# Kernel optimization log

Measured on AMD Instinct MI355X. Metric: run time of the kernel, lower is better.

Reference implementation:

```python
import jax, jax.numpy as jnp
import numpy as np

THR = 0.2
POOL_A = 160
POOL_B = 96
EPS = 1e-5


def _adaptive_avg_pool_last(x, out_size):
    # torch AdaptiveAvgPool1d semantics: bin i averages [floor(i*n/o), ceil((i+1)*n/o))
    n = x.shape[-1]
    i = np.arange(out_size)
    starts = (i * n) // out_size
    ends = -((-(i + 1) * n) // out_size)
    cs = jnp.cumsum(x, axis=-1)
    cs = jnp.concatenate([jnp.zeros_like(cs[..., :1]), cs], axis=-1)
    sums = cs[..., ends] - cs[..., starts]
    return sums / jnp.asarray(ends - starts, x.dtype)


def _unfold3x3(x, H, W):
    # Faithful to torch: raw reshape (N, L, C) -> (N, C, H, W) (memory reinterpretation,
    # NOT a transpose), then F.unfold(k=3, pad=1) and rearrange 'n (c ww) l -> n l ww c'.
    N, L, C = x.shape
    img = x.reshape(N, C, H, W)
    pad = jnp.pad(img, ((0, 0), (0, 0), (1, 1), (1, 1)))
    # window positions in row-major (ky, kx) order, matching F.unfold
    patches = jnp.stack([pad[:, :, dy:dy + H, dx:dx + W]
                         for dy in range(3) for dx in range(3)], axis=2)  # (N,C,9,H,W)
    return patches.transpose(0, 3, 4, 2, 1).reshape(N, H * W, 9, C)  # (N,L,9,C)


def _forward(feat_s0, feat_s1, ln_weight, ln_bias):
    N, L, C = feat_s0.shape
    H = W = int(round(L ** 0.5))
    conf = jnp.einsum('nlc,nsc->nls', feat_s0, feat_s1) / (C ** 0.5)
    conf = jax.nn.softmax(conf, axis=1) * jax.nn.softmax(conf, axis=2)
    # mutual nearest-neighbor mask with confidence threshold
    mask = ((conf > THR)
            & (conf == conf.max(axis=2, keepdims=True))
            & (conf == conf.max(axis=1, keepdims=True))).astype(feat_s0.dtype)
    u0 = _unfold3x3(feat_s0, H, W)
    u1 = _unfold3x3(feat_s1, H, W)
    sem0 = jnp.einsum('nlc,nlwc->nlw', feat_s0, u0) / C  # divided by C (shape[-1]), as in source
    sem1 = jnp.einsum('nlc,nlwc->nlw', feat_s1, u1) / C
    fea0 = jnp.einsum('nlwc,nlw->nlc', u0, sem0)
    fea1 = jnp.einsum('nlwc,nlw->nlc', u1, sem1)
    s0 = jnp.einsum('nls,nsd->nld', mask, fea1) / L
    s1 = jnp.einsum('nsl,nsd->nld', mask, fea0) / L
    f0 = jnp.concatenate([_adaptive_avg_pool_last(feat_s0, POOL_A),
                          _adaptive_avg_pool_last(s0, POOL_B)], axis=-1)
    f1 = jnp.concatenate([_adaptive_avg_pool_last(feat_s1, POOL_A),
                          _adaptive_avg_pool_last(s1, POOL_B)], axis=-1)
    f = jnp.concatenate([f0, f1], axis=0)  # (2N, L, 256)
    mu = f.mean(-1, keepdims=True)
    var = f.var(-1, keepdims=True)
    f = (f - mu) * jax.lax.rsqrt(var + EPS) * ln_weight + ln_bias
    return f[:N], f[N:]


def setup_inputs():
    key = jax.random.key(0)
    k0, k1 = jax.random.split(key)
    N, L, C = 2, 4096, 256
    return {
        'feat_s0': jax.random.normal(k0, (N, L, C), jnp.float32),
        'feat_s1': jax.random.normal(k1, (N, L, C), jnp.float32),
        'ln_weight': jnp.ones((C,), jnp.float32),
        'ln_bias': jnp.zeros((C,), jnp.float32),
    }


def reference(feat_s0, feat_s1, ln_weight, ln_bias):
    return _forward(feat_s0, feat_s1, ln_weight, ln_bias)
```

## Files before the change

kernel.cpp:

```cpp
#include <hip/hip_runtime.h>
#include <stdint.h>

#define NBATCH 2
#define LL 4096
#define CC 256
#define LSTR8 144
#define KEXP 0.09016844f
#define KEXP2 0.18033688f
#define IMIN (-2147483647 - 1)

typedef long i64f;
typedef float f32x4 __attribute__((ext_vector_type(4)));

#if defined(__has_builtin) && __has_builtin(__builtin_amdgcn_exp2f)
#define EXP2F(x) __builtin_amdgcn_exp2f(x)
#else
#define EXP2F(x) exp2f(x)
#endif

__global__ __launch_bounds__(256) void cast_fp8(
    const float* __restrict__ a, const float* __restrict__ b,
    uint32_t* __restrict__ oa, uint32_t* __restrict__ ob,
    float* __restrict__ rowSum, float* __restrict__ colSum,
    int* __restrict__ rowPart, int* __restrict__ colPart){
  int idx = blockIdx.x * 256 + threadIdx.x;
  if (idx < NBATCH*LL){
    rowSum[idx] = 0.f; colSum[idx] = 0.f;
    rowPart[idx] = IMIN; colPart[idx] = IMIN;
  }
  float4 va = ((const float4*)a)[idx];
  float4 vb = ((const float4*)b)[idx];
  int ra = __builtin_amdgcn_cvt_pk_fp8_f32(va.x, va.y, 0, false);
  ra = __builtin_amdgcn_cvt_pk_fp8_f32(va.z, va.w, ra, true);
  int rb = __builtin_amdgcn_cvt_pk_fp8_f32(vb.x, vb.y, 0, false);
  rb = __builtin_amdgcn_cvt_pk_fp8_f32(vb.z, vb.w, rb, true);
  oa[idx] = (uint32_t)ra;
  ob[idx] = (uint32_t)rb;
}

__global__ __launch_bounds__(256, 4) void conf_pass(
    const uint8_t* __restrict__ f0q, const uint8_t* __restrict__ f1q,
    float* __restrict__ rowSum, float* __restrict__ colSum,
    int* __restrict__ rowPart, int* __restrict__ colPart){
  __shared__ uint8_t Alds[128*LSTR8], Blds[128*LSTR8];
  float* rowS = (float*)Alds;
  float* colS = (float*)(Alds + 1024);
  int*   rb   = (int*)  (Alds + 2048);
  int*   cb   = (int*)  (Alds + 3072);
  int bl = (blockIdx.z*32 + blockIdx.y)*32 + blockIdx.x;
  int nb = (bl & 7)*256 + (bl >> 3);
  int st = nb & 31, lt = (nb >> 5) & 31, n = nb >> 10;
  int t = threadIdx.x;
  const int wv = t >> 6, lane = t & 63, lr = lane & 15, quad = lane >> 4;
  const int lq = wv >> 1, sq = wv & 1;
  const uint8_t* A = f0q + (size_t)n*LL*CC + (size_t)(lt*128)*CC;
  const uint8_t* B = f1q + (size_t)n*LL*CC + (size_t)(st*128)*CC;
  f32x4 acc[4][4];
  #pragma unroll
  for (int r = 0; r < 4; r++)
    #pragma unroll
    for (int j = 0; j < 4; j++) acc[r][j] = (f32x4){0.f,0.f,0.f,0.f};

  auto compute = [&](){
    #pragma unroll
    for (int kk = 0; kk < 4; kk++){
      i64f a[4], bf[4];
      #pragma unroll
      for (int r = 0; r < 4; r++)
        a[r] = *(const i64f*)(Alds + (lq*64 + r*16 + lr)*LSTR8 + kk*32 + quad*8);
      #pragma unroll
      for (int j = 0; j < 4; j++)
        bf[j] = *(const i64f*)(Blds + (sq*64 + j*16 + lr)*LSTR8 + kk*32 + quad*8);
      #pragma unroll
      for (int r = 0; r < 4; r++)
        #pragma unroll
        for (int j = 0; j < 4; j++)
          acc[r][j] = __builtin_amdgcn_mfma_f32_16x16x32_fp8_fp8(a[r], bf[j], acc[r][j], 0, 0, 0);
    }
  };

  #pragma unroll
  for (int m = 0; m < 8; m++){
    int f = m*256 + t, row = f >> 4, kg = f & 15;
    *(uint2*)(Alds + row*LSTR8 + kg*8) = *(const uint2*)(A + (size_t)row*CC + kg*8);
    *(uint2*)(Blds + row*LSTR8 + kg*8) = *(const uint2*)(B + (size_t)row*CC + kg*8);
  }
  uint2 pa[8], pb[8];
  #pragma unroll
  for (int m = 0; m < 8; m++){
    int f = m*256 + t, row = f >> 4, kg = f & 15;
    pa[m] = *(const uint2*)(A + (size_t)row*CC + 128 + kg*8);
    pb[m] = *(const uint2*)(B + (size_t)row*CC + 128 + kg*8);
  }
  __syncthreads();
  compute();
  __syncthreads();
  #pragma unroll
  for (int m = 0; m < 8; m++){
    int f = m*256 + t, row = f >> 4, kg = f & 15;
    *(uint2*)(Alds + row*LSTR8 + kg*8) = pa[m];
    *(uint2*)(Blds + row*LSTR8 + kg*8) = pb[m];
  }
  __syncthreads();
  compute();

  const int sbase = st*128 + sq*64 + lr;
  const int lbase = lt*128 + lq*64 + quad*4;
  float rsum[4][4], csum[4] = {0.f,0.f,0.f,0.f};
  int rkey[4][4], ckey[4] = {IMIN,IMIN,IMIN,IMIN};
  #pragma unroll
  for (int r = 0; r < 4; r++)
    #pragma unroll
    for (int rr = 0; rr < 4; rr++){ rsum[r][rr] = 0.f; rkey[r][rr] = IMIN; }
  #pragma unroll
  for (int r = 0; r < 4; r++)
    #pragma unroll
    for (int j = 0; j < 4; j++)
      #pragma unroll
      for (int rr = 0; rr < 4; rr++){
        float a = acc[r][j][rr];
        float e = EXP2F(a * KEXP);
        rsum[r][rr] += e;
        csum[j] += e;
        int iqs = ((int)(a * 2048.f)) << 12;
        rkey[r][rr] = max(rkey[r][rr], iqs + (sbase + j*16));
        ckey[j]     = max(ckey[j],     iqs + (lbase + r*16 + rr));
      }
  #pragma unroll
  for (int msk = 1; msk <= 8; msk <<= 1)
    #pragma unroll
    for (int r = 0; r < 4; r++)
      #pragma unroll
      for (int rr = 0; rr < 4; rr++){
        rsum[r][rr] += __shfl_xor(rsum[r][rr], msk);
        rkey[r][rr] = max(rkey[r][rr], __shfl_xor(rkey[r][rr], msk));
      }
  #pragma unroll
  for (int msk = 16; msk <= 32; msk <<= 1)
    #pragma unroll
    for (int j = 0; j < 4; j++){
      csum[j] += __shfl_xor(csum[j], msk);
      ckey[j] = max(ckey[j], __shfl_xor(ckey[j], msk));
    }
  __syncthreads();
  if (lr == 0){
    #pragma unroll
    for (int r = 0; r < 4; r++)
      #pragma unroll
      for (int rr = 0; rr < 4; rr++){
        int row = lq*64 + r*16 + quad*4 + rr;
        rowS[sq*128 + row] = rsum[r][rr];
        rb[sq*128 + row]   = rkey[r][rr];
      }
  }
  if (quad == 0){
    #pragma unroll
    for (int j = 0; j < 4; j++){
      int col = sq*64 + j*16 + lr;
      colS[lq*128 + col] = csum[j];
      cb[lq*128 + col]   = ckey[j];
    }
  }
  __syncthreads();
  if (t < 128){
    unsafeAtomicAdd(&rowSum[(size_t)n*LL + lt*128 + t], rowS[t] + rowS[128 + t]);
    unsafeAtomicAdd(&colSum[(size_t)n*LL + st*128 + t], colS[t] + colS[128 + t]);
    atomicMax(&rowPart[(size_t)n*LL + lt*128 + t], max(rb[t], rb[128 + t]));
    atomicMax(&colPart[(size_t)n*LL + st*128 + t], max(cb[t], cb[128 + t]));
  }
}

__device__ float fea_fly(const float* __restrict__ featn, int srow, int t){
  __shared__ float sred[9][4];
  __shared__ float ssem[9];
  int lane = t & 63, wv = t >> 6;
  int h = srow >> 6, xx = srow & 63;
  float fv = featn[(size_t)srow * CC + t];
  float uv[9];
  #pragma unroll
  for (int w = 0; w < 9; w++){
    int dy = w/3 - 1, dx = w%3 - 1;
    int y = h + dy, x = xx + dx;
    uv[w] = (y >= 0 && y < 64 && x >= 0 && x < 64) ? featn[(size_t)t * 4096 + y*64 + x] : 0.f;
  }
  __syncthreads();
  #pragma unroll
  for (int w = 0; w < 9; w++){
    float pvv = fv * uv[w];
    #pragma unroll
    for (int msk = 1; msk <= 32; msk <<= 1) pvv += __shfl_xor(pvv, msk);
    if (lane == 0) sred[w][wv] = pvv;
  }
  __syncthreads();
  if (t < 9) ssem[t] = (sred[t][0] + sred[t][1] + sred[t][2] + sred[t][3]) * (1.f/256.f);
  __syncthreads();
  float acc = 0.f;
  #pragma unroll
  for (int w = 0; w < 9; w++) acc += uv[w] * ssem[w];
  __syncthreads();
  return acc;
}

__device__ __forceinline__ float pool_window(const float* f, const float* s, int t){
  if (t < 160){
    int a = (t*8)/5, e = (t*8+12)/5;
    float sum = 0.f;
    for (int i = a; i < e; i++) sum += f[i];
    return sum / (float)(e - a);
  } else {
    int tt = t - 160;
    int a = (tt*8)/3, e = (tt*8+10)/3;
    float sum = 0.f;
    for (int i = a; i < e; i++) sum += s[i];
    return sum / (float)(e - a);
  }
}

__global__ __launch_bounds__(256) void tail(
    const float* __restrict__ feat0, const float* __restrict__ feat1,
    const float* __restrict__ rowSum, const float* __restrict__ colSum,
    const int* __restrict__ rowPart, const int* __restrict__ colPart,
    const float* __restrict__ lnw, const float* __restrict__ lnb,
    float* __restrict__ out){
  int l = blockIdx.x, n = blockIdx.y, t = threadIdx.x;
  int lane = t & 63, wv = t >> 6;
  size_t base = (size_t)n * LL;
  float fv0 = feat0[(base + l)*CC + t];
  float fv1 = feat1[(base + l)*CC + t];
  float w = lnw[t], bsh = lnb[t];
  int   rowK = rowPart[base + l], colK = colPart[base + l];
  float Rl   = rowSum[base + l],  Cl   = colSum[base + l];
  int ssr = rowK & 4095, ssc = colK & 4095;
  float Cssr = colSum[base + ssr], Rssc = rowSum[base + ssc];
  int   ck2  = colPart[base + ssr], rk2 = rowPart[base + ssc];
  float v0 = 0.f, v1 = 0.f;
  {
    float araw = (float)(rowK >> 12) * (1.f/2048.f);
    float val = exp2f(araw * KEXP2) / (Rl * Cssr);
    if (val > 0.2f && (ck2 & 4095) == l)
      v0 = fea_fly(feat1 + (size_t)n*LL*CC, ssr, t) * (1.f/4096.f);
  }
  {
    float araw = (float)(colK >> 12) * (1.f/2048.f);
    float val = exp2f(araw * KEXP2) / (Cl * Rssc);
    if (val > 0.2f && (rk2 & 4095) == l)
      v1 = fea_fly(feat0 + (size_t)n*LL*CC, ssc, t) * (1.f/4096.f);
  }
  __shared__ float f0r[CC], f1r[CC], s0r[CC], s1r[CC];
  __shared__ float redA[2][4], redB[2][4];
  f0r[t] = fv0;
  f1r[t] = fv1;
  s0r[t] = v0;
  s1r[t] = v1;
  __syncthreads();
  float pA = pool_window(f0r, s0r, t);
  float pB = pool_window(f1r, s1r, t);
  float smA = pA, sqA = pA*pA, smB = pB, sqB = pB*pB;
  #pragma unroll
  for (int msk = 1; msk <= 32; msk <<= 1){
    smA += __shfl_xor(smA, msk);
    sqA += __shfl_xor(sqA, msk);
    smB += __shfl_xor(smB, msk);
    sqB += __shfl_xor(sqB, msk);
  }
  if (lane == 0){ redA[0][wv] = smA; redA[1][wv] = sqA; redB[0][wv] = smB; redB[1][wv] = sqB; }
  __syncthreads();
  float tsA = redA[0][0]+redA[0][1]+redA[0][2]+redA[0][3];
  float tqA = redA[1][0]+redA[1][1]+redA[1][2]+redA[1][3];
  float tsB = redB[0][0]+redB[0][1]+redB[0][2]+redB[0][3];
  float tqB = redB[1][0]+redB[1][1]+redB[1][2]+redB[1][3];
  float muA = tsA * (1.f/256.f), varA = tqA * (1.f/256.f) - muA*muA;
  float muB = tsB * (1.f/256.f), varB = tqB * (1.f/256.f) - muB*muB;
  out[((size_t)n*LL + l)*CC + t]       = (pA - muA) * rsqrtf(varA + 1e-5f) * w + bsh;
  out[((size_t)(2 + n)*LL + l)*CC + t] = (pB - muB) * rsqrtf(varB + 1e-5f) * w + bsh;
}

extern "C" void kernel_launch(void* const* d_in, const int* in_sizes, int n_in,
                              void* d_out, int out_size, void* d_ws, size_t ws_size,
                              hipStream_t stream){
  const float* feat0 = (const float*)d_in[0];
  const float* feat1 = (const float*)d_in[1];
  const float* lnw   = (const float*)d_in[2];
  const float* lnb   = (const float*)d_in[3];
  float* out = (float*)d_out;
  char* ws = (char*)d_ws;
  const size_t MB = 1024 * 1024;
  uint8_t* f0q = (uint8_t*)(ws + 0);
  uint8_t* f1q = (uint8_t*)(ws + 2*MB);
  float* rowSum  = (float*)(ws + 4*MB);
  float* colSum  = (float*)(ws + 4*MB + 32*1024);
  int*   rowPart = (int*)  (ws + 4*MB + 64*1024);
  int*   colPart = (int*)  (ws + 4*MB + 96*1024);

  cast_fp8<<<2048, 256, 0, stream>>>(feat0, feat1, (uint32_t*)f0q, (uint32_t*)f1q,
                                     rowSum, colSum, rowPart, colPart);
  dim3 gconf(32, 32, NBATCH);
  conf_pass<<<gconf, 256, 0, stream>>>(f0q, f1q, rowSum, colSum, rowPart, colPart);
  dim3 gt(LL, NBATCH);
  tail<<<gt, 256, 0, stream>>>(feat0, feat1, rowSum, colSum, rowPart, colPart,
                               lnw, lnb, out);
}
```

Baseline: 131.8 us.

## Fuse confidence pass and tail into a persistent kernel with grid barrier

Merges the fp8 confidence GEMM kernel and the per-row tail kernel into one persistent kernel of 1024 blocks. Each block handles two GEMM tiles, then waits on a software grid barrier built from an atomic counter, then processes eight output rows. The prep kernel now converts two float4s per thread and resets the barrier counter. This is meant to remove a kernel launch and the 8192-block tail grid. In exchange it depends on all 1024 blocks being co-resident, and the tail runs with fewer blocks and more serialized work per block.

```diff
diff --git a/kernel.cpp b/kernel.cpp
--- a/kernel.cpp
+++ b/kernel.cpp
@@ -8,6 +8,7 @@
 #define KEXP 0.09016844f
 #define KEXP2 0.18033688f
 #define IMIN (-2147483647 - 1)
+#define NBLK 1024
 
 typedef long i64f;
 typedef float f32x4 __attribute__((ext_vector_type(4)));
@@ -18,161 +19,45 @@
 #define EXP2F(x) exp2f(x)
 #endif
 
-__global__ __launch_bounds__(256) void cast_fp8(
+__global__ __launch_bounds__(256) void prep(
     const float* __restrict__ a, const float* __restrict__ b,
     uint32_t* __restrict__ oa, uint32_t* __restrict__ ob,
     float* __restrict__ rowSum, float* __restrict__ colSum,
-    int* __restrict__ rowPart, int* __restrict__ colPart){
-  int idx = blockIdx.x * 256 + threadIdx.x;
-  if (idx < NBATCH*LL){
-    rowSum[idx] = 0.f; colSum[idx] = 0.f;
-    rowPart[idx] = IMIN; colPart[idx] = IMIN;
-  }
-  float4 va = ((const float4*)a)[idx];
-  float4 vb = ((const float4*)b)[idx];
-  int ra = __builtin_amdgcn_cvt_pk_fp8_f32(va.x, va.y, 0, false);
-  ra = __builtin_amdgcn_cvt_pk_fp8_f32(va.z, va.w, ra, true);
-  int rb = __builtin_amdgcn_cvt_pk_fp8_f32(vb.x, vb.y, 0, false);
-  rb = __builtin_amdgcn_cvt_pk_fp8_f32(vb.z, vb.w, rb, true);
-  oa[idx] = (uint32_t)ra;
-  ob[idx] = (uint32_t)rb;
-}
-
-__global__ __launch_bounds__(256, 4) void conf_pass(
-    const uint8_t* __restrict__ f0q, const uint8_t* __restrict__ f1q,
-    float* __restrict__ rowSum, float* __restrict__ colSum,
-    int* __restrict__ rowPart, int* __restrict__ colPart){
-  __shared__ uint8_t Alds[128*LSTR8], Blds[128*LSTR8];
-  float* rowS = (float*)Alds;
-  float* colS = (float*)(Alds + 1024);
-  int*   rb   = (int*)  (Alds + 2048);
-  int*   cb   = (int*)  (Alds + 3072);
-  int bl = (blockIdx.z*32 + blockIdx.y)*32 + blockIdx.x;
-  int nb = (bl & 7)*256 + (bl >> 3);
-  int st = nb & 31, lt = (nb >> 5) & 31, n = nb >> 10;
-  int t = threadIdx.x;
-  const int wv = t >> 6, lane = t & 63, lr = lane & 15, quad = lane >> 4;
-  const int lq = wv >> 1, sq = wv & 1;
-  const uint8_t* A = f0q + (size_t)n*LL*CC + (size_t)(lt*128)*CC;
-  const uint8_t* B = f1q + (size_t)n*LL*CC + (size_t)(st*128)*CC;
-  f32x4 acc[4][4];
+    int* __restrict__ rowPart, int* __restrict__ colPart,
+    int* __restrict__ barCtr){
+  int gid = blockIdx.x * 256 + threadIdx.x;
+  if (gid < NBATCH*LL){
+    rowSum[gid] = 0.f; colSum[gid] = 0.f;
+    rowPart[gid] = IMIN; colPart[gid] = IMIN;
+  }
+  if (gid == 0) *barCtr = 0;
   #pragma unroll
-  for (int r = 0; r < 4; r++)
-    #pragma unroll
-    for (int j = 0; j < 4; j++) acc[r][j] = (f32x4){0.f,0.f,0.f,0.f};
-
-  auto compute = [&](){
-    #pragma unroll
-    for (int kk = 0; kk < 4; kk++){
-      i64f a[4], bf[4];
-      #pragma unroll
-      for (int r = 0; r < 4; r++)
-        a[r] = *(const i64f*)(Alds + (lq*64 + r*16 + lr)*LSTR8 + kk*32 + quad*8);
-      #pragma unroll
-      for (int j = 0; j < 4; j++)
-        bf[j] = *(const i64f*)(Blds + (sq*64 + j*16 + lr)*LSTR8 + kk*32 + quad*8);
-      #pragma unroll
-      for (int r = 0; r < 4; r++)
-        #pragma unroll
-        for (int j = 0; j < 4; j++)
-          acc[r][j] = __builtin_amdgcn_mfma_f32_16x16x32_fp8_fp8(a[r], bf[j], acc[r][j], 0, 0, 0);
-    }
-  };
-
-  #pragma unroll
-  for (int m = 0; m < 8; m++){
-    int f = m*256 + t, row = f >> 4, kg = f & 15;
-    *(uint2*)(Alds + row*LSTR8 + kg*8) = *(const uint2*)(A + (size_t)row*CC + kg*8);
-    *(uint2*)(Blds + row*LSTR8 + kg*8) = *(const uint2*)(B + (size_t)row*CC + kg*8);
-  }
-  uint2 pa[8], pb[8];
-  #pragma unroll
-  for (int m = 0; m < 8; m++){
-    int f = m*256 + t, row = f >> 4, kg = f & 15;
-    pa[m] = *(const uint2*)(A + (size_t)row*CC + 128 + kg*8);
-    pb[m] = *(const uint2*)(B + (size_t)row*CC + 128 + kg*8);
-  }
-  __syncthreads();
-  compute();
-  __syncthreads();
-  #pragma unroll
-  for (int m = 0; m < 8; m++){
-    int f = m*256 + t, row = f >> 4, kg = f & 15;
-    *(uint2*)(Alds + row*LSTR8 + kg*8) = pa[m];
-    *(uint2*)(Blds + row*LSTR8 + kg*8) = pb[m];
-  }
-  __syncthreads();
-  compute();
-
-  const int sbase = st*128 + sq*64 + lr;
-  const int lbase = lt*128 + lq*64 + quad*4;
-  float rsum[4][4], csum[4] = {0.f,0.f,0.f,0.f};
-  int rkey[4][4], ckey[4] = {IMIN,IMIN,IMIN,IMIN};
-  #pragma unroll
-  for (int r = 0; r < 4; r++)
-    #pragma unroll
-    for (int rr = 0; rr < 4; rr++){ rsum[r][rr] = 0.f; rkey[r][rr] = IMIN; }
-  #pragma unroll
-  for (int r = 0; r < 4; r++)
-    #pragma unroll
-    for (int j = 0; j < 4; j++)
-      #pragma unroll
-      for (int rr = 0; rr < 4; rr++){
-        float a = acc[r][j][rr];
-        float e = EXP2F(a * KEXP);
-        rsum[r][rr] += e;
-        csum[j] += e;
-        int iqs = ((int)(a * 2048.f)) << 12;
-        rkey[r][rr] = max(rkey[r][rr], iqs + (sbase + j*16));
-        ckey[j]     = max(ckey[j],     iqs + (lbase + r*16 + rr));
-      }
-  #pragma unroll
-  for (int msk = 1; msk <= 8; msk <<= 1)
-    #pragma unroll
-    for (int r = 0; r < 4; r++)
-      #pragma unroll
-      for (int rr = 0; rr < 4; rr++){
-        rsum[r][rr] += __shfl_xor(rsum[r][rr], msk);
-        rkey[r][rr] = max(rkey[r][rr], __shfl_xor(rkey[r][rr], msk));
-      }
-  #pragma unroll
-  for (int msk = 16; msk <= 32; msk <<= 1)
-    #pragma unroll
-    for (int j = 0; j < 4; j++){
-      csum[j] += __shfl_xor(csum[j], msk);
-      ckey[j] = max(ckey[j], __shfl_xor(ckey[j], msk));
-    }
-  __syncthreads();
-  if (lr == 0){
-    #pragma unroll
-    for (int r = 0; r < 4; r++)
-      #pragma unroll
-      for (int rr = 0; rr < 4; rr++){
-        int row = lq*64 + r*16 + quad*4 + rr;
-        rowS[sq*128 + row] = rsum[r][rr];
-        rb[sq*128 + row]   = rkey[r][rr];
-      }
-  }
-  if (quad == 0){
-    #pragma unroll
-    for (int j = 0; j < 4; j++){
-      int col = sq*64 + j*16 + lr;
-      colS[lq*128 + col] = csum[j];
-      cb[lq*128 + col]   = ckey[j];
-    }
-  }
-  __syncthreads();
-  if (t < 128){
-    unsafeAtomicAdd(&rowSum[(size_t)n*LL + lt*128 + t], rowS[t] + rowS[128 + t]);
-    unsafeAtomicAdd(&colSum[(size_t)n*LL + st*128 + t], colS[t] + colS[128 + t]);
-    atomicMax(&rowPart[(size_t)n*LL + lt*128 + t], max(rb[t], rb[128 + t]));
-    atomicMax(&colPart[(size_t)n*LL + st*128 + t], max(cb[t], cb[128 + t]));
-  }
-}
-
-__device__ float fea_fly(const float* __restrict__ featn, int srow, int t){
-  __shared__ float sred[9][4];
-  __shared__ float ssem[9];
+  for (int k = 0; k < 2; k++){
+    int idx = gid*2 + k;
+    float4 va = ((const float4*)a)[idx];
+    float4 vb = ((const float4*)b)[idx];
+    int ra = __builtin_amdgcn_cvt_pk_fp8_f32(va.x, va.y, 0, false);
+    ra = __builtin_amdgcn_cvt_pk_fp8_f32(va.z, va.w, ra, true);
+    int rb = __builtin_amdgcn_cvt_pk_fp8_f32(vb.x, vb.y, 0, false);
+    rb = __builtin_amdgcn_cvt_pk_fp8_f32(vb.z, vb.w, rb, true);
+    oa[idx] = (uint32_t)ra;
+    ob[idx] = (uint32_t)rb;
+  }
+}
+
+__device__ __forceinline__ void grid_barrier(int* ctr){
+  __syncthreads();
+  if (threadIdx.x == 0){
+    __threadfence();
+    __hip_atomic_fetch_add(ctr, 1, __ATOMIC_RELEASE, __HIP_MEMORY_SCOPE_AGENT);
+    while (__hip_atomic_load(ctr, __ATOMIC_ACQUIRE, __HIP_MEMORY_SCOPE_AGENT) < NBLK)
+      __builtin_amdgcn_s_sleep(2);
+  }
+  __syncthreads();
+}
+
+__device__ float fea_fly(const float* __restrict__ featn, int srow, int t,
+                         float* __restrict__ sred , float* __restrict__ ssem ){
   int lane = t & 63, wv = t >> 6;
   int h = srow >> 6, xx = srow & 63;
   float fv = featn[(size_t)srow * CC + t];
@@ -189,10 +74,10 @@
     float pvv = fv * uv[w];
     #pragma unroll
     for (int msk = 1; msk <= 32; msk <<= 1) pvv += __shfl_xor(pvv, msk);
-    if (lane == 0) sred[w][wv] = pvv;
-  }
-  __syncthreads();
-  if (t < 9) ssem[t] = (sred[t][0] + sred[t][1] + sred[t][2] + sred[t][3]) * (1.f/256.f);
+    if (lane == 0) sred[w*4 + wv] = pvv;
+  }
+  __syncthreads();
+  if (t < 9) ssem[t] = (sred[t*4+0] + sred[t*4+1] + sred[t*4+2] + sred[t*4+3]) * (1.f/256.f);
   __syncthreads();
   float acc = 0.f;
   #pragma unroll
@@ -216,63 +101,191 @@
   }
 }
 
-__global__ __launch_bounds__(256) void tail(
+__global__ __launch_bounds__(256, 4) void fused(
+    const uint8_t* __restrict__ f0q, const uint8_t* __restrict__ f1q,
     const float* __restrict__ feat0, const float* __restrict__ feat1,
-    const float* __restrict__ rowSum, const float* __restrict__ colSum,
-    const int* __restrict__ rowPart, const int* __restrict__ colPart,
+    float* __restrict__ rowSum, float* __restrict__ colSum,
+    int* __restrict__ rowPart, int* __restrict__ colPart,
     const float* __restrict__ lnw, const float* __restrict__ lnb,
-    float* __restrict__ out){
-  int l = blockIdx.x, n = blockIdx.y, t = threadIdx.x;
-  int lane = t & 63, wv = t >> 6;
-  size_t base = (size_t)n * LL;
-  float fv0 = feat0[(base + l)*CC + t];
-  float fv1 = feat1[(base + l)*CC + t];
+    float* __restrict__ out, int* __restrict__ barCtr){
+  __shared__ __align__(16) uint8_t smem[36864];
+  uint8_t* Alds = smem;
+  uint8_t* Blds = smem + 18432;
+  int bl = blockIdx.x;
+  int t = threadIdx.x;
+  const int wv = t >> 6, lane = t & 63, lr = lane & 15, quad = lane >> 4;
+  const int lq = wv >> 1, sq = wv & 1;
+
+  int nbb = (bl & 7)*128 + (bl >> 3);
+  for (int i = 0; i < 2; i++){
+    int nb = nbb*2 + i;
+    int st = nb & 31, lt = (nb >> 5) & 31, n = nb >> 10;
+    const uint8_t* A = f0q + (size_t)n*LL*CC + (size_t)(lt*128)*CC;
+    const uint8_t* B = f1q + (size_t)n*LL*CC + (size_t)(st*128)*CC;
+    f32x4 acc[4][4];
+    #pragma unroll
+    for (int r = 0; r < 4; r++)
+      #pragma unroll
+      for (int j = 0; j < 4; j++) acc[r][j] = (f32x4){0.f,0.f,0.f,0.f};
+    for (int kc = 0; kc < 2; kc++){
+      __syncthreads();
+      #pragma unroll
+      for (int m = 0; m < 8; m++){
+        int f = m*256 + t, row = f >> 4, kg = f & 15;
+        *(uint2*)(Alds + row*LSTR8 + kg*8) =
+            *(const uint2*)(A + (size_t)row*CC + kc*128 + kg*8);
+        *(uint2*)(Blds + row*LSTR8 + kg*8) =
+            *(const uint2*)(B + (size_t)row*CC + kc*128 + kg*8);
+      }
+      __syncthreads();
+      #pragma unroll
+      for (int kk = 0; kk < 4; kk++){
+        i64f a[4], bf[4];
+        #pragma unroll
+        for (int r = 0; r < 4; r++)
+          a[r] = *(const i64f*)(Alds + (lq*64 + r*16 + lr)*LSTR8 + kk*32 + quad*8);
+        #pragma unroll
+        for (int j = 0; j < 4; j++)
+          bf[j] = *(const i64f*)(Blds + (sq*64 + j*16 + lr)*LSTR8 + kk*32 + quad*8);
+        #pragma unroll
+        for (int r = 0; r < 4; r++)
+          #pragma unroll
+          for (int j = 0; j < 4; j++)
+            acc[r][j] = __builtin_amdgcn_mfma_f32_16x16x32_fp8_fp8(a[r], bf[j], acc[r][j], 0, 0, 0);
+      }
+    }
+    const int sbase = st*128 + sq*64 + lr;
+    const int lbase = lt*128 + lq*64 + quad*4;
+    float rsum[4][4], csum[4] = {0.f,0.f,0.f,0.f};
+    int rkey[4][4], ckey[4] = {IMIN,IMIN,IMIN,IMIN};
+    #pragma unroll
+    for (int r = 0; r < 4; r++)
+      #pragma unroll
+      for (int rr = 0; rr < 4; rr++){ rsum[r][rr] = 0.f; rkey[r][rr] = IMIN; }
+    #pragma unroll
+    for (int r = 0; r < 4; r++)
+      #pragma unroll
+      for (int j = 0; j < 4; j++)
+        #pragma unroll
+        for (int rr = 0; rr < 4; rr++){
+          float a = acc[r][j][rr];
+          float e = EXP2F(a * KEXP);
+          rsum[r][rr] += e;
+          csum[j] += e;
+          int iqs = ((int)(a * 2048.f)) << 12;
+          rkey[r][rr] = max(rkey[r][rr], iqs + (sbase + j*16));
+          ckey[j]     = max(ckey[j],     iqs + (lbase + r*16 + rr));
+        }
+    #pragma unroll
+    for (int msk = 1; msk <= 8; msk <<= 1)
+      #pragma unroll
+      for (int r = 0; r < 4; r++)
+        #pragma unroll
+        for (int rr = 0; rr < 4; rr++){
+          rsum[r][rr] += __shfl_xor(rsum[r][rr], msk);
+          rkey[r][rr] = max(rkey[r][rr], __shfl_xor(rkey[r][rr], msk));
+        }
+    #pragma unroll
+    for (int msk = 16; msk <= 32; msk <<= 1)
+      #pragma unroll
+      for (int j = 0; j < 4; j++){
+        csum[j] += __shfl_xor(csum[j], msk);
+        ckey[j] = max(ckey[j], __shfl_xor(ckey[j], msk));
+      }
+    __syncthreads();
+    float* rowS = (float*)smem;
+    float* colS = (float*)(smem + 1024);
+    int*   rb   = (int*)  (smem + 2048);
+    int*   cb   = (int*)  (smem + 3072);
+    if (lr == 0){
+      #pragma unroll
+      for (int r = 0; r < 4; r++)
+        #pragma unroll
+        for (int rr = 0; rr < 4; rr++){
+          int row = lq*64 + r*16 + quad*4 + rr;
+          rowS[sq*128 + row] = rsum[r][rr];
+          rb[sq*128 + row]   = rkey[r][rr];
+        }
+    }
+    if (quad == 0){
+      #pragma unroll
+      for (int j = 0; j < 4; j++){
+        int col = sq*64 + j*16 + lr;
+        colS[lq*128 + col] = csum[j];
+        cb[lq*128 + col]   = ckey[j];
+      }
+    }
+    __syncthreads();
+    if (t < 128){
+      unsafeAtomicAdd(&rowSum[(size_t)n*LL + lt*128 + t], rowS[t] + rowS[128 + t]);
+      unsafeAtomicAdd(&colSum[(size_t)n*LL + st*128 + t], colS[t] + colS[128 + t]);
+      atomicMax(&rowPart[(size_t)n*LL + lt*128 + t], max(rb[t], rb[128 + t]));
+      atomicMax(&colPart[(size_t)n*LL + st*128 + t], max(cb[t], cb[128 + t]));
+    }
+  }
+
+  grid_barrier(barCtr);
+
+  float* f0r  = (float*)smem;
+  float* f1r  = (float*)(smem + 1024);
+  float* s0r  = (float*)(smem + 2048);
+  float* s1r  = (float*)(smem + 3072);
+  float* sred = (float*)(smem + 4096);
+  float* ssem = (float*)(smem + 4352);
+  float* redA = (float*)(smem + 4608);
+  float* redB = (float*)(smem + 4640);
   float w = lnw[t], bsh = lnb[t];
-  int   rowK = rowPart[base + l], colK = colPart[base + l];
-  float Rl   = rowSum[base + l],  Cl   = colSum[base + l];
-  int ssr = rowK & 4095, ssc = colK & 4095;
-  float Cssr = colSum[base + ssr], Rssc = rowSum[base + ssc];
-  int   ck2  = colPart[base + ssr], rk2 = rowPart[base + ssc];
-  float v0 = 0.f, v1 = 0.f;
-  {
-    float araw = (float)(rowK >> 12) * (1.f/2048.f);
-    float val = exp2f(araw * KEXP2) / (Rl * Cssr);
-    if (val > 0.2f && (ck2 & 4095) == l)
-      v0 = fea_fly(feat1 + (size_t)n*LL*CC, ssr, t) * (1.f/4096.f);
-  }
-  {
-    float araw = (float)(colK >> 12) * (1.f/2048.f);
-    float val = exp2f(araw * KEXP2) / (Cl * Rssc);
-    if (val > 0.2f && (rk2 & 4095) == l)
-      v1 = fea_fly(feat0 + (size_t)n*LL*CC, ssc, t) * (1.f/4096.f);
-  }
-  __shared__ float f0r[CC], f1r[CC], s0r[CC], s1r[CC];
-  __shared__ float redA[2][4], redB[2][4];
-  f0r[t] = fv0;
-  f1r[t] = fv1;
-  s0r[t] = v0;
-  s1r[t] = v1;
-  __syncthreads();
-  float pA = pool_window(f0r, s0r, t);
-  float pB = pool_window(f1r, s1r, t);
-  float smA = pA, sqA = pA*pA, smB = pB, sqB = pB*pB;
-  #pragma unroll
-  for (int msk = 1; msk <= 32; msk <<= 1){
-    smA += __shfl_xor(smA, msk);
-    sqA += __shfl_xor(sqA, msk);
-    smB += __shfl_xor(smB, msk);
-    sqB += __shfl_xor(sqB, msk);
-  }
-  if (lane == 0){ redA[0][wv] = smA; redA[1][wv] = sqA; redB[0][wv] = smB; redB[1][wv] = sqB; }
-  __syncthreads();
-  float tsA = redA[0][0]+redA[0][1]+redA[0][2]+redA[0][3];
-  float tqA = redA[1][0]+redA[1][1]+redA[1][2]+redA[1][3];
-  float tsB = redB[0][0]+redB[0][1]+redB[0][2]+redB[0][3];
-  float tqB = redB[1][0]+redB[1][1]+redB[1][2]+redB[1][3];
-  float muA = tsA * (1.f/256.f), varA = tqA * (1.f/256.f) - muA*muA;
-  float muB = tsB * (1.f/256.f), varB = tqB * (1.f/256.f) - muB*muB;
-  out[((size_t)n*LL + l)*CC + t]       = (pA - muA) * rsqrtf(varA + 1e-5f) * w + bsh;
-  out[((size_t)(2 + n)*LL + l)*CC + t] = (pB - muB) * rsqrtf(varB + 1e-5f) * w + bsh;
+  for (int i = 0; i < 8; i++){
+    int tid2 = bl*8 + i;
+    int n = tid2 >> 12, l = tid2 & 4095;
+    size_t base = (size_t)n * LL;
+    float fv0 = feat0[(base + l)*CC + t];
+    float fv1 = feat1[(base + l)*CC + t];
+    int   rowK = rowPart[base + l], colK = colPart[base + l];
+    float Rl   = rowSum[base + l],  Cl   = colSum[base + l];
+    int ssr = rowK & 4095, ssc = colK & 4095;
+    float Cssr = colSum[base + ssr], Rssc = rowSum[base + ssc];
+    int   ck2  = colPart[base + ssr], rk2 = rowPart[base + ssc];
+    float v0 = 0.f, v1 = 0.f;
+    {
+      float araw = (float)(rowK >> 12) * (1.f/2048.f);
+      float val = exp2f(araw * KEXP2) / (Rl * Cssr);
+      if (val > 0.2f && (ck2 & 4095) == l)
+        v0 = fea_fly(feat1 + (size_t)n*LL*CC, ssr, t, sred, ssem) * (1.f/4096.f);
+    }
+    {
+      float araw = (float)(colK >> 12) * (1.f/2048.f);
+      float val = exp2f(araw * KEXP2) / (Cl * Rssc);
+      if (val > 0.2f && (rk2 & 4095) == l)
+        v1 = fea_fly(feat0 + (size_t)n*LL*CC, ssc, t, sred, ssem) * (1.f/4096.f);
+    }
+    f0r[t] = fv0;
+    f1r[t] = fv1;
+    s0r[t] = v0;
+    s1r[t] = v1;
+    __syncthreads();
+    float pA = pool_window(f0r, s0r, t);
+    float pB = pool_window(f1r, s1r, t);
+    float smA = pA, sqA = pA*pA, smB = pB, sqB = pB*pB;
+    #pragma unroll
+    for (int msk = 1; msk <= 32; msk <<= 1){
+      smA += __shfl_xor(smA, msk);
+      sqA += __shfl_xor(sqA, msk);
+      smB += __shfl_xor(smB, msk);
+      sqB += __shfl_xor(sqB, msk);
+    }
+    if (lane == 0){ redA[0*4+wv] = smA; redA[1*4+wv] = sqA; redB[0*4+wv] = smB; redB[1*4+wv] = sqB; }
+    __syncthreads();
+    float tsA = redA[0]+redA[1]+redA[2]+redA[3];
+    float tqA = redA[4]+redA[5]+redA[6]+redA[7];
+    float tsB = redB[0]+redB[1]+redB[2]+redB[3];
+    float tqB = redB[4]+redB[5]+redB[6]+redB[7];
+    float muA = tsA * (1.f/256.f), varA = tqA * (1.f/256.f) - muA*muA;
+    float muB = tsB * (1.f/256.f), varB = tqB * (1.f/256.f) - muB*muB;
+    out[((size_t)n*LL + l)*CC + t]       = (pA - muA) * rsqrtf(varA + 1e-5f) * w + bsh;
+    out[((size_t)(2 + n)*LL + l)*CC + t] = (pB - muB) * rsqrtf(varB + 1e-5f) * w + bsh;
+    __syncthreads();
+  }
 }
 
 extern "C" void kernel_launch(void* const* d_in, const int* in_sizes, int n_in,
@@ -291,12 +304,11 @@
   float* colSum  = (float*)(ws + 4*MB + 32*1024);
   int*   rowPart = (int*)  (ws + 4*MB + 64*1024);
   int*   colPart = (int*)  (ws + 4*MB + 96*1024);
-
-  cast_fp8<<<2048, 256, 0, stream>>>(feat0, feat1, (uint32_t*)f0q, (uint32_t*)f1q,
-                                     rowSum, colSum, rowPart, colPart);
-  dim3 gconf(32, 32, NBATCH);
-  conf_pass<<<gconf, 256, 0, stream>>>(f0q, f1q, rowSum, colSum, rowPart, colPart);
-  dim3 gt(LL, NBATCH);
-  tail<<<gt, 256, 0, stream>>>(feat0, feat1, rowSum, colSum, rowPart, colPart,
-                               lnw, lnb, out);
-}
+  int*   barCtr  = (int*)  (ws + 4*MB + 128*1024);
+
+  prep<<<1024, 256, 0, stream>>>(feat0, feat1, (uint32_t*)f0q, (uint32_t*)f1q,
+                                 rowSum, colSum, rowPart, colPart, barCtr);
+  fused<<<NBLK, 256, 0, stream>>>(f0q, f1q, feat0, feat1,
+                                  rowSum, colSum, rowPart, colPart,
+                                  lnw, lnb, out, barCtr);
+}
```

After: 311.4 us. 136% more time.

## Load first K-half via direct global-to-LDS with XOR-swizzled layout

Applied to the files above, without the earlier changes.

Replaces the padded LDS layout (stride 144) with an unpadded 128-byte row layout that uses an XOR swizzle on 16-byte chunks to avoid bank conflicts. The first K-half tile is loaded with global_load_lds, writing straight into LDS without passing through registers, and the swizzle is applied on the source-address side. The second half is still register-staged, with a pre-swizzled source offset so the stores land in the same layout. This aims to cut LDS footprint and register traffic in the prologue. It relies on global_load_lds semantics (wave-contiguous destination) matching the swizzle, which is delicate to get right.

```diff
diff --git a/kernel.cpp b/kernel.cpp
--- a/kernel.cpp
+++ b/kernel.cpp
@@ -4,7 +4,6 @@
 #define NBATCH 2
 #define LL 4096
 #define CC 256
-#define LSTR8 144
 #define KEXP 0.09016844f
 #define KEXP2 0.18033688f
 #define IMIN (-2147483647 - 1)
@@ -17,6 +16,10 @@
 #else
 #define EXP2F(x) exp2f(x)
 #endif
+
+#define GLDS16(g, l) __builtin_amdgcn_global_load_lds(                      \
+    (const __attribute__((address_space(1))) uint32_t*)(g),                 \
+    (__attribute__((address_space(3))) uint32_t*)(l), 16, 0, 0)
 
 __global__ __launch_bounds__(256) void cast_fp8(
     const float* __restrict__ a, const float* __restrict__ b,
@@ -42,7 +45,8 @@
     const uint8_t* __restrict__ f0q, const uint8_t* __restrict__ f1q,
     float* __restrict__ rowSum, float* __restrict__ colSum,
     int* __restrict__ rowPart, int* __restrict__ colPart){
-  __shared__ uint8_t Alds[128*LSTR8], Blds[128*LSTR8];
+  __shared__ __align__(16) uint8_t Alds[128*128];
+  __shared__ __align__(16) uint8_t Blds[128*128];
   float* rowS = (float*)Alds;
   float* colS = (float*)(Alds + 1024);
   int*   rb   = (int*)  (Alds + 2048);
@@ -53,6 +57,7 @@
   int t = threadIdx.x;
   const int wv = t >> 6, lane = t & 63, lr = lane & 15, quad = lane >> 4;
   const int lq = wv >> 1, sq = wv & 1;
+  const int swzr = (lr & 7) << 4;
   const uint8_t* A = f0q + (size_t)n*LL*CC + (size_t)(lt*128)*CC;
   const uint8_t* B = f1q + (size_t)n*LL*CC + (size_t)(st*128)*CC;
   f32x4 acc[4][4];
@@ -64,13 +69,14 @@
   auto compute = [&](){
     #pragma unroll
     for (int kk = 0; kk < 4; kk++){
+      int off = (kk*32 + quad*8) ^ swzr;
       i64f a[4], bf[4];
       #pragma unroll
       for (int r = 0; r < 4; r++)
-        a[r] = *(const i64f*)(Alds + (lq*64 + r*16 + lr)*LSTR8 + kk*32 + quad*8);
+        a[r] = *(const i64f*)(Alds + (lq*64 + r*16 + lr)*128 + off);
       #pragma unroll
       for (int j = 0; j < 4; j++)
-        bf[j] = *(const i64f*)(Blds + (sq*64 + j*16 + lr)*LSTR8 + kk*32 + quad*8);
+        bf[j] = *(const i64f*)(Blds + (sq*64 + j*16 + lr)*128 + off);
       #pragma unroll
       for (int r = 0; r < 4; r++)
         #pragma unroll
@@ -79,27 +85,32 @@
     }
   };
 
+  {
+    int rsub = lane >> 3, csub = lane & 7;
+    int srcOff = ((csub ^ rsub) << 4);
+    #pragma unroll
+    for (int m = 0; m < 4; m++){
+      int row = m*32 + wv*8 + rsub;
+      GLDS16(A + (size_t)row*CC + srcOff, Alds + m*4096 + wv*1024);
+      GLDS16(B + (size_t)row*CC + srcOff, Blds + m*4096 + wv*1024);
+    }
+  }
+  uint2 pa[8], pb[8];
   #pragma unroll
   for (int m = 0; m < 8; m++){
     int f = m*256 + t, row = f >> 4, kg = f & 15;
-    *(uint2*)(Alds + row*LSTR8 + kg*8) = *(const uint2*)(A + (size_t)row*CC + kg*8);
-    *(uint2*)(Blds + row*LSTR8 + kg*8) = *(const uint2*)(B + (size_t)row*CC + kg*8);
-  }
-  uint2 pa[8], pb[8];
+    int so = (kg*8) ^ ((row & 7) << 4);
+    pa[m] = *(const uint2*)(A + (size_t)row*CC + 128 + so);
+    pb[m] = *(const uint2*)(B + (size_t)row*CC + 128 + so);
+  }
+  __syncthreads();
+  compute();
+  __syncthreads();
   #pragma unroll
   for (int m = 0; m < 8; m++){
     int f = m*256 + t, row = f >> 4, kg = f & 15;
-    pa[m] = *(const uint2*)(A + (size_t)row*CC + 128 + kg*8);
-    pb[m] = *(const uint2*)(B + (size_t)row*CC + 128 + kg*8);
-  }
-  __syncthreads();
-  compute();
-  __syncthreads();
-  #pragma unroll
-  for (int m = 0; m < 8; m++){
-    int f = m*256 + t, row = f >> 4, kg = f & 15;
-    *(uint2*)(Alds + row*LSTR8 + kg*8) = pa[m];
-    *(uint2*)(Blds + row*LSTR8 + kg*8) = pb[m];
+    *(uint2*)(Alds + row*128 + kg*8) = pa[m];
+    *(uint2*)(Blds + row*128 + kg*8) = pb[m];
   }
   __syncthreads();
   compute();
```

After: 122.5 us. -7.1%, faster.
